# Optimization experiments

Measured on AMD Instinct MI355X. Metric: run time of the kernel, lower is better.

The kernel has to match this reference:

```python
import jax, jax.numpy as jnp
import numpy as np

H = 64  # latent_dim // 2


def _lstm_cell(x, h, c, Wih, Whh, b):
    # PyTorch gate order: i, f, g, o
    g = x @ Wih.T + h @ Whh.T + b
    i, f, gg, o = jnp.split(g, 4, axis=-1)
    c = jax.nn.sigmoid(f) * c + jax.nn.sigmoid(i) * jnp.tanh(gg)
    h = jax.nn.sigmoid(o) * jnp.tanh(c)
    return h, c


def _run_lstm(x, Wih, Whh, b):
    # x: [B, T, D] -> outputs [B, T, H], final h, c (zero-initialized state)
    B = x.shape[0]
    h0 = jnp.zeros((B, Whh.shape[1]), x.dtype)

    def step(carry, xt):
        h, c = _lstm_cell(xt, carry[0], carry[1], Wih, Whh, b)
        return (h, c), h

    (h, c), ys = jax.lax.scan(step, (h0, h0), jnp.swapaxes(x, 0, 1))
    return jnp.swapaxes(ys, 0, 1), h, c


def setup_inputs() -> dict:
    key = jax.random.key(0)
    ks = jax.random.split(key, 16)
    B, S, T, D = 512, 1024, 512, 3
    s = 1.0 / np.sqrt(H)

    def u(k, shape):
        return jax.random.uniform(k, shape, jnp.float32, -s, s)

    return {
        "src": jax.random.normal(ks[0], (B, S, D), jnp.float32),
        "trg": jax.random.normal(ks[1], (B, T, D), jnp.float32),
        "enc1_Wih": u(ks[2], (4 * H, D)),
        "enc1_Whh": u(ks[3], (4 * H, H)),
        "enc1_b": u(ks[4], (4 * H,)),
        "enc2_Wih": u(ks[5], (4 * H, H)),
        "enc2_Whh": u(ks[6], (4 * H, H)),
        "enc2_b": u(ks[7], (4 * H,)),
        "dec1_Wih": u(ks[8], (4 * H, D)),
        "dec1_Whh": u(ks[9], (4 * H, H)),
        "dec1_b": u(ks[10], (4 * H,)),
        "dec2_Wih": u(ks[11], (4 * H, H)),
        "dec2_Whh": u(ks[12], (4 * H, H)),
        "dec2_b": u(ks[13], (4 * H,)),
        "fc_W": u(ks[14], (D, H)),
        "fc_b": u(ks[15], (D,)),
    }


def reference(src, trg, enc1_Wih, enc1_Whh, enc1_b, enc2_Wih, enc2_Whh, enc2_b,
              dec1_Wih, dec1_Whh, dec1_b, dec2_Wih, dec2_Whh, dec2_b, fc_W, fc_b):
    # Encoder: two stacked LSTMs over src; keep final state of layer 2.
    y1, _, _ = _run_lstm(src, enc1_Wih, enc1_Whh, enc1_b)
    _, h, c = _run_lstm(y1, enc2_Wih, enc2_Whh, enc2_b)

    # Decoder (teacher_forcing_ratio = 1.0, the only well-defined branch):
    # at each step both decoder LSTMs share/chain the SAME (h, c) state,
    # exactly as the original Decoder.forward does with seq-len-1 inputs.
    def step(carry, xt):
        h, c = carry
        h1, c1 = _lstm_cell(xt, h, c, dec1_Wih, dec1_Whh, dec1_b)
        h2, c2 = _lstm_cell(h1, h1, c1, dec2_Wih, dec2_Whh, dec2_b)
        return (h2, c2), h2 @ fc_W.T + fc_b

    xs = jnp.swapaxes(trg[:, :-1, :], 0, 1)  # inputs for t = 1..T-1
    _, preds = jax.lax.scan(step, (h, c), xs)
    preds = jnp.swapaxes(preds, 0, 1)  # [B, T-1, 3]

    B = trg.shape[0]
    zero0 = jnp.zeros((B, 1, fc_b.shape[0]), preds.dtype)  # outputs[:, 0] stays 0
    return jnp.concatenate([zero0, preds], axis=1)
```

## Files before the change

kernel.cpp:

```cpp
#include <hip/hip_runtime.h>
#include <math.h>

typedef _Float16 f16;
typedef _Float16 f16x8 __attribute__((ext_vector_type(8)));
typedef float    f32x4 __attribute__((ext_vector_type(4)));

#define MFMA16(A, B, C) __builtin_amdgcn_mfma_f32_16x16x32_f16((A), (B), (C), 0, 0, 0)
#define LOG2E 1.44269504088896f

__device__ __forceinline__ float sig2(float a) {
    return __builtin_amdgcn_rcpf(1.0f + __builtin_amdgcn_exp2f(a));
}
__device__ __forceinline__ float tanh2(float c) {
    return fmaf(2.0f, sig2(c * (-2.0f * LOG2E)), -1.0f);
}

__device__ __forceinline__ f16x8 ldfrag(const float* __restrict__ W, int n, int k0, float s) {
    const float* p = W + (size_t)n * 64 + k0;
    f16x8 r;
#pragma unroll
    for (int j = 0; j < 8; j++) r[j] = (f16)(s * p[j]);
    return r;
}

__global__ __launch_bounds__(512, 2)
void seq2seq_kernel(const float* __restrict__ src, const float* __restrict__ trg,
                    const float* __restrict__ e1ih, const float* __restrict__ e1hh,
                    const float* __restrict__ e1b,
                    const float* __restrict__ e2ih, const float* __restrict__ e2hh,
                    const float* __restrict__ e2b,
                    const float* __restrict__ d1ih, const float* __restrict__ d1hh,
                    const float* __restrict__ d1b,
                    const float* __restrict__ d2ih, const float* __restrict__ d2hh,
                    const float* __restrict__ d2b,
                    const float* __restrict__ fcW, const float* __restrict__ fcb,
                    float* __restrict__ out)
{
    const int bp   = blockIdx.x;
    const int tid  = threadIdx.x;
    const int wv   = tid >> 6;
    const bool isB = (wv >= 4);
    const int wvg  = wv & 3;
    const int lane = tid & 63;
    const int quad = lane >> 4;
    const int c15  = lane & 15;
    const int u16  = wvg * 16 + c15;
    const int qb   = quad & 1;
    const int ab   = c15 & 1;

    __shared__ __align__(16) float xst[1024][8];
    __shared__ __align__(16) float tst[512][8];
    __shared__ __align__(16) f16 h1l[2][2][64];
    __shared__ __align__(16) f16 h2l[2][2][64];
    __shared__ float c1buf[2][64];
    __shared__ float c2buf[2][64];

    {
        const float* s0 = src + (size_t)(2 * bp) * 3072;
        const float* s1 = s0 + 3072;
        for (int i = tid; i < 3072; i += 512) {
            int t = i / 3, c = i - 3 * t;
            xst[t][c]     = s0[i];
            xst[t][4 + c] = s1[i];
        }
        const float* t0p = trg + (size_t)(2 * bp) * 1536;
        const float* t1p = t0p + 1536;
        for (int i = tid; i < 1536; i += 512) {
            int t = i / 3, c = i - 3 * t;
            tst[t][c]     = t0p[i];
            tst[t][4 + c] = t1p[i];
        }
    }

    f16x8 E1hh[4][2];
    f16x8 E2ih[4][2], E2hh[4][2];
    float xw[4][3], bias1[4], bias2[4];
    if (!isB) {
#pragma unroll
        for (int g = 0; g < 4; g++) {
            const float s = (g == 2) ? (-2.0f * LOG2E) : (-LOG2E);
            const int n = g * 64 + u16;
#pragma unroll
            for (int c = 0; c < 2; c++)
                E1hh[g][c] = ldfrag(e1hh, n, c * 32 + quad * 8, s);
            xw[g][0] = s * e1ih[n * 3 + 0];
            xw[g][1] = s * e1ih[n * 3 + 1];
            xw[g][2] = s * e1ih[n * 3 + 2];
            bias1[g] = s * e1b[n];
        }
    } else {
#pragma unroll
        for (int g = 0; g < 4; g++) {
            const float s = (g == 2) ? (-2.0f * LOG2E) : (-LOG2E);
            const int n = g * 64 + u16;
#pragma unroll
            for (int c = 0; c < 2; c++) {
                E2ih[g][c] = ldfrag(e2ih, n, c * 32 + quad * 8, s);
                E2hh[g][c] = ldfrag(e2hh, n, c * 32 + quad * 8, s);
            }
            bias2[g] = s * e2b[n];
        }
    }

    float c1 = 0.f, c2 = 0.f;
    if (tid < 256) {
        (&h1l[0][0][0])[tid] = (f16)0.f;
        (&h2l[0][0][0])[tid] = (f16)0.f;
    }
    __syncthreads();

    const f32x4 z4 = {0.f, 0.f, 0.f, 0.f};

#pragma unroll 1
    for (int tau = 0; tau <= 1024; tau++) {
        const int w = tau & 1;
        if (!isB) {
            if (tau < 1024) {
                const f32x4 xv = *(const f32x4*)&xst[tau][qb * 4];
                const f16* h1p = h1l[w ^ 1][ab];
                f16x8 a0 = *(const f16x8*)(h1p + quad * 8);
                f16x8 a1 = *(const f16x8*)(h1p + 32 + quad * 8);
                float xt[4];
#pragma unroll
                for (int g = 0; g < 4; g++)
                    xt[g] = fmaf(xw[g][0], xv.x,
                            fmaf(xw[g][1], xv.y, fmaf(xw[g][2], xv.z, bias1[g])));
                f32x4 acc[4];
#pragma unroll
                for (int g = 0; g < 4; g++)
                    acc[g] = MFMA16(a1, E1hh[g][1], MFMA16(a0, E1hh[g][0], z4));
                float v[4];
#pragma unroll
                for (int g = 0; g < 4; g++)
                    v[g] = (qb ? acc[g][1] : acc[g][0]) + xt[g];
                float iv = sig2(v[0]), fv = sig2(v[1]);
                float gv = fmaf(2.0f, sig2(v[2]), -1.0f), ov = sig2(v[3]);
                c1 = fv * c1 + iv * gv;
                if (quad < 2) h1l[w][quad][u16] = (f16)(ov * tanh2(c1));
            }
        } else {
            if (tau > 0) {
                const f16* h1p = h1l[w ^ 1][ab];
                const f16* h2p = h2l[w ^ 1][ab];
                f16x8 a0 = *(const f16x8*)(h1p + quad * 8);
                f16x8 a1 = *(const f16x8*)(h1p + 32 + quad * 8);
                f16x8 b0 = *(const f16x8*)(h2p + quad * 8);
                f16x8 b1 = *(const f16x8*)(h2p + 32 + quad * 8);
                f32x4 accA[4], accB[4];
#pragma unroll
                for (int g = 0; g < 4; g++) {
                    accA[g] = MFMA16(a1, E2ih[g][1], MFMA16(a0, E2ih[g][0], z4));
                    accB[g] = MFMA16(b1, E2hh[g][1], MFMA16(b0, E2hh[g][0], z4));
                }
                float v[4];
#pragma unroll
                for (int g = 0; g < 4; g++)
                    v[g] = (qb ? accA[g][1] : accA[g][0]) +
                           (qb ? accB[g][1] : accB[g][0]) + bias2[g];
                float iv = sig2(v[0]), fv = sig2(v[1]);
                float gv = fmaf(2.0f, sig2(v[2]), -1.0f), ov = sig2(v[3]);
                c2 = fv * c2 + iv * gv;
                if (quad < 2) h2l[w][quad][u16] = (f16)(ov * tanh2(c2));
            }
        }
        __syncthreads();
    }

    f16x8 D1hh[4][2];
    f16x8 W2s[4][2];
    float dxw[4][3], db1[4], db2[4];
    if (!isB) {
#pragma unroll
        for (int g = 0; g < 4; g++) {
            const float s = (g == 2) ? (-2.0f * LOG2E) : (-LOG2E);
            const int n = g * 64 + u16;
#pragma unroll
            for (int c = 0; c < 2; c++)
                D1hh[g][c] = ldfrag(d1hh, n, c * 32 + quad * 8, s);
            dxw[g][0] = s * d1ih[n * 3 + 0];
            dxw[g][1] = s * d1ih[n * 3 + 1];
            dxw[g][2] = s * d1ih[n * 3 + 2];
            db1[g] = s * d1b[n];
        }
    } else {
#pragma unroll
        for (int g = 0; g < 4; g++) {
            const float s = (g == 2) ? (-2.0f * LOG2E) : (-LOG2E);
            const int n = g * 64 + u16;
#pragma unroll
            for (int c = 0; c < 2; c++) {
                const int k0 = c * 32 + quad * 8;
                const float* pa = d2ih + (size_t)n * 64 + k0;
                const float* pb = d2hh + (size_t)n * 64 + k0;
                f16x8 r;
#pragma unroll
                for (int j = 0; j < 8; j++) r[j] = (f16)(s * (pa[j] + pb[j]));
                W2s[g][c] = r;
            }
            db2[g] = s * d2b[n];
        }
        if (quad < 2) c2buf[quad][u16] = c2;
    }
    float fw0 = 0.f, fw1 = 0.f, fw2 = 0.f;
    float fb0 = fcb[0], fb1 = fcb[1], fb2 = fcb[2];
    if (wv >= 6) { fw0 = fcW[lane]; fw1 = fcW[64 + lane]; fw2 = fcW[128 + lane]; }
    __syncthreads();

#pragma unroll 1
    for (int t = 0; t < 511; t++) {
        const int r = t & 1, w = r ^ 1;
        if (!isB) {
            const f16* hp = h2l[r][ab];
            f16x8 a0 = *(const f16x8*)(hp + quad * 8);
            f16x8 a1 = *(const f16x8*)(hp + 32 + quad * 8);
            const f32x4 xv = *(const f32x4*)&tst[t][qb * 4];
            float cdin = c2buf[qb][u16];
            float xt[4];
#pragma unroll
            for (int g = 0; g < 4; g++)
                xt[g] = fmaf(dxw[g][0], xv.x,
                        fmaf(dxw[g][1], xv.y, fmaf(dxw[g][2], xv.z, db1[g])));
            f32x4 acc[4];
#pragma unroll
            for (int g = 0; g < 4; g++)
                acc[g] = MFMA16(a1, D1hh[g][1], MFMA16(a0, D1hh[g][0], z4));
            float v[4];
#pragma unroll
            for (int g = 0; g < 4; g++)
                v[g] = (qb ? acc[g][1] : acc[g][0]) + xt[g];
            float iv = sig2(v[0]), fv = sig2(v[1]);
            float gv = fmaf(2.0f, sig2(v[2]), -1.0f), ov = sig2(v[3]);
            float c1d = fv * cdin + iv * gv;
            if (quad < 2) {
                h1l[w][quad][u16] = (f16)(ov * tanh2(c1d));
                c1buf[quad][u16]  = c1d;
            }
        } else if (wv >= 6 && t > 0) {
            const int bsel = wv - 6;
            float hv = (float)h2l[r][bsel][lane];
            float p0 = fw0 * hv, p1 = fw1 * hv, p2 = fw2 * hv;
#pragma unroll
            for (int off = 32; off > 0; off >>= 1) {
                p0 += __shfl_down(p0, off);
                p1 += __shfl_down(p1, off);
                p2 += __shfl_down(p2, off);
            }
            if (lane == 0) {
                float* o = out + ((size_t)(2 * bp + bsel) * 512 + t) * 3;
                o[0] = p0 + fb0; o[1] = p1 + fb1; o[2] = p2 + fb2;
            }
        }
        __syncthreads();

        if (isB) {
            const f16* np = h1l[w][ab];
            f16x8 m0 = *(const f16x8*)(np + quad * 8);
            f16x8 m1 = *(const f16x8*)(np + 32 + quad * 8);
            float c1in = c1buf[qb][u16];
            f32x4 acc[4];
#pragma unroll
            for (int g = 0; g < 4; g++)
                acc[g] = MFMA16(m1, W2s[g][1], MFMA16(m0, W2s[g][0], z4));
            float v[4];
#pragma unroll
            for (int g = 0; g < 4; g++)
                v[g] = (qb ? acc[g][1] : acc[g][0]) + db2[g];
            float i2 = sig2(v[0]), f2 = sig2(v[1]);
            float g2 = fmaf(2.0f, sig2(v[2]), -1.0f), o2 = sig2(v[3]);
            float c2d = f2 * c1in + i2 * g2;
            if (quad < 2) {
                h2l[w][quad][u16] = (f16)(o2 * tanh2(c2d));
                c2buf[quad][u16]  = c2d;
            }
        }
        __syncthreads();
    }

    if (wv >= 6) {
        const int bsel = wv - 6;
        float hv = (float)h2l[1][bsel][lane];
        float p0 = fw0 * hv, p1 = fw1 * hv, p2 = fw2 * hv;
#pragma unroll
        for (int off = 32; off > 0; off >>= 1) {
            p0 += __shfl_down(p0, off);
            p1 += __shfl_down(p1, off);
            p2 += __shfl_down(p2, off);
        }
        if (lane == 0) {
            float* o = out + ((size_t)(2 * bp + bsel) * 512 + 511) * 3;
            o[0] = p0 + fb0; o[1] = p1 + fb1; o[2] = p2 + fb2;
        }
    }
}

extern "C" void kernel_launch(void* const* d_in, const int* in_sizes, int n_in,
                              void* d_out, int out_size, void* d_ws, size_t ws_size,
                              hipStream_t stream)
{
    const float* src   = (const float*)d_in[0];
    const float* trg   = (const float*)d_in[1];
    const float* e1ih  = (const float*)d_in[2];
    const float* e1hh  = (const float*)d_in[3];
    const float* e1b   = (const float*)d_in[4];
    const float* e2ih  = (const float*)d_in[5];
    const float* e2hh  = (const float*)d_in[6];
    const float* e2b   = (const float*)d_in[7];
    const float* dd1ih = (const float*)d_in[8];
    const float* dd1hh = (const float*)d_in[9];
    const float* dd1b  = (const float*)d_in[10];
    const float* dd2ih = (const float*)d_in[11];
    const float* dd2hh = (const float*)d_in[12];
    const float* dd2b  = (const float*)d_in[13];
    const float* fcW   = (const float*)d_in[14];
    const float* fcb   = (const float*)d_in[15];
    float* out = (float*)d_out;

    hipMemsetAsync(d_out, 0, (size_t)out_size * sizeof(float), stream);

    seq2seq_kernel<<<256, 512, 0, stream>>>(src, trg,
                                            e1ih, e1hh, e1b, e2ih, e2hh, e2b,
                                            dd1ih, dd1hh, dd1b, dd2ih, dd2hh, dd2b,
                                            fcW, fcb, out);
}
```

Measured before the change: 926.0 us.

## Batch FC output via ring buffer MFMA, prefetch inputs, fold biases into MFMA

Decoder h2 outputs are written into a 16-step shared ring buffer, and the final linear layer is computed every 16 steps with one MFMA instead of a per-step shuffle reduction. Next-step input features are prefetched into registers before the barrier. Layer-2 biases are folded into the MFMA accumulator initialisation. This cuts per-step latency on the serial critical path but adds an fp16 FC projection and more complex indexing at the boundaries.

```diff
diff --git a/kernel.cpp b/kernel.cpp
--- a/kernel.cpp
+++ b/kernel.cpp
@@ -54,6 +54,7 @@
     __shared__ __align__(16) f16 h2l[2][2][64];
     __shared__ float c1buf[2][64];
     __shared__ float c2buf[2][64];
+    __shared__ __align__(16) f16 ring[2][16][72];
 
     {
         const float* s0 = src + (size_t)(2 * bp) * 3072;
@@ -74,7 +75,8 @@
 
     f16x8 E1hh[4][2];
     f16x8 E2ih[4][2], E2hh[4][2];
-    float xw[4][3], bias1[4], bias2[4];
+    float xw[4][3], bias1[4];
+    f32x4 bs2[4];
     if (!isB) {
 #pragma unroll
         for (int g = 0; g < 4; g++) {
@@ -98,7 +100,8 @@
                 E2ih[g][c] = ldfrag(e2ih, n, c * 32 + quad * 8, s);
                 E2hh[g][c] = ldfrag(e2hh, n, c * 32 + quad * 8, s);
             }
-            bias2[g] = s * e2b[n];
+            float bv = s * e2b[n];
+            bs2[g] = (f32x4){bv, bv, bv, bv};
         }
     }
 
@@ -110,21 +113,23 @@
     __syncthreads();
 
     const f32x4 z4 = {0.f, 0.f, 0.f, 0.f};
+
+    f32x4 xq = z4, xnq = z4;
+    if (!isB) xq = *(const f32x4*)&xst[0][qb * 4];
 
 #pragma unroll 1
     for (int tau = 0; tau <= 1024; tau++) {
         const int w = tau & 1;
         if (!isB) {
             if (tau < 1024) {
-                const f32x4 xv = *(const f32x4*)&xst[tau][qb * 4];
                 const f16* h1p = h1l[w ^ 1][ab];
                 f16x8 a0 = *(const f16x8*)(h1p + quad * 8);
                 f16x8 a1 = *(const f16x8*)(h1p + 32 + quad * 8);
                 float xt[4];
 #pragma unroll
                 for (int g = 0; g < 4; g++)
-                    xt[g] = fmaf(xw[g][0], xv.x,
-                            fmaf(xw[g][1], xv.y, fmaf(xw[g][2], xv.z, bias1[g])));
+                    xt[g] = fmaf(xw[g][0], xq.x,
+                            fmaf(xw[g][1], xq.y, fmaf(xw[g][2], xq.z, bias1[g])));
                 f32x4 acc[4];
 #pragma unroll
                 for (int g = 0; g < 4; g++)
@@ -137,6 +142,8 @@
                 float gv = fmaf(2.0f, sig2(v[2]), -1.0f), ov = sig2(v[3]);
                 c1 = fv * c1 + iv * gv;
                 if (quad < 2) h1l[w][quad][u16] = (f16)(ov * tanh2(c1));
+                const int tn = (tau + 1 < 1024) ? tau + 1 : 1023;
+                xnq = *(const f32x4*)&xst[tn][qb * 4];
             }
         } else {
             if (tau > 0) {
@@ -149,14 +156,14 @@
                 f32x4 accA[4], accB[4];
 #pragma unroll
                 for (int g = 0; g < 4; g++) {
-                    accA[g] = MFMA16(a1, E2ih[g][1], MFMA16(a0, E2ih[g][0], z4));
+                    accA[g] = MFMA16(a1, E2ih[g][1], MFMA16(a0, E2ih[g][0], bs2[g]));
                     accB[g] = MFMA16(b1, E2hh[g][1], MFMA16(b0, E2hh[g][0], z4));
                 }
                 float v[4];
 #pragma unroll
                 for (int g = 0; g < 4; g++)
                     v[g] = (qb ? accA[g][1] : accA[g][0]) +
-                           (qb ? accB[g][1] : accB[g][0]) + bias2[g];
+                           (qb ? accB[g][1] : accB[g][0]);
                 float iv = sig2(v[0]), fv = sig2(v[1]);
                 float gv = fmaf(2.0f, sig2(v[2]), -1.0f), ov = sig2(v[3]);
                 c2 = fv * c2 + iv * gv;
@@ -164,11 +171,13 @@
             }
         }
         __syncthreads();
+        if (!isB) xq = xnq;
     }
 
     f16x8 D1hh[4][2];
     f16x8 W2s[4][2];
-    float dxw[4][3], db1[4], db2[4];
+    float dxw[4][3], db1[4];
+    f32x4 db2s[4];
     if (!isB) {
 #pragma unroll
         for (int g = 0; g < 4; g++) {
@@ -197,14 +206,25 @@
                 for (int j = 0; j < 8; j++) r[j] = (f16)(s * (pa[j] + pb[j]));
                 W2s[g][c] = r;
             }
-            db2[g] = s * d2b[n];
+            float bv = s * d2b[n];
+            db2s[g] = (f32x4){bv, bv, bv, bv};
         }
         if (quad < 2) c2buf[quad][u16] = c2;
     }
-    float fw0 = 0.f, fw1 = 0.f, fw2 = 0.f;
-    float fb0 = fcb[0], fb1 = fcb[1], fb2 = fcb[2];
-    if (wv >= 6) { fw0 = fcW[lane]; fw1 = fcW[64 + lane]; fw2 = fcW[128 + lane]; }
+    f16x8 FW0 = {}, FW1 = {};
+    float fb = 0.f;
+    if (wv >= 6 && c15 < 3) {
+#pragma unroll
+        for (int j = 0; j < 8; j++) {
+            FW0[j] = (f16)fcW[c15 * 64 + quad * 8 + j];
+            FW1[j] = (f16)fcW[c15 * 64 + 32 + quad * 8 + j];
+        }
+        fb = fcb[c15];
+    }
     __syncthreads();
+
+    f32x4 tq = z4, tnq = z4;
+    if (!isB) tq = *(const f32x4*)&tst[0][qb * 4];
 
 #pragma unroll 1
     for (int t = 0; t < 511; t++) {
@@ -213,13 +233,12 @@
             const f16* hp = h2l[r][ab];
             f16x8 a0 = *(const f16x8*)(hp + quad * 8);
             f16x8 a1 = *(const f16x8*)(hp + 32 + quad * 8);
-            const f32x4 xv = *(const f32x4*)&tst[t][qb * 4];
             float cdin = c2buf[qb][u16];
             float xt[4];
 #pragma unroll
             for (int g = 0; g < 4; g++)
-                xt[g] = fmaf(dxw[g][0], xv.x,
-                        fmaf(dxw[g][1], xv.y, fmaf(dxw[g][2], xv.z, db1[g])));
+                xt[g] = fmaf(dxw[g][0], tq.x,
+                        fmaf(dxw[g][1], tq.y, fmaf(dxw[g][2], tq.z, db1[g])));
             f32x4 acc[4];
 #pragma unroll
             for (int g = 0; g < 4; g++)
@@ -235,22 +254,23 @@
                 h1l[w][quad][u16] = (f16)(ov * tanh2(c1d));
                 c1buf[quad][u16]  = c1d;
             }
-        } else if (wv >= 6 && t > 0) {
+            const int tn = (t + 1 < 511) ? t + 1 : 510;
+            tnq = *(const f32x4*)&tst[tn][qb * 4];
+        } else if (wv >= 6 && t > 0 && (t & 15) == 0) {
             const int bsel = wv - 6;
-            float hv = (float)h2l[r][bsel][lane];
-            float p0 = fw0 * hv, p1 = fw1 * hv, p2 = fw2 * hv;
-#pragma unroll
-            for (int off = 32; off > 0; off >>= 1) {
-                p0 += __shfl_down(p0, off);
-                p1 += __shfl_down(p1, off);
-                p2 += __shfl_down(p2, off);
-            }
-            if (lane == 0) {
-                float* o = out + ((size_t)(2 * bp + bsel) * 512 + t) * 3;
-                o[0] = p0 + fb0; o[1] = p1 + fb1; o[2] = p2 + fb2;
+            const f16* rp = &ring[bsel][0][0];
+            f16x8 fa0 = *(const f16x8*)(rp + c15 * 72 + quad * 8);
+            f16x8 fa1 = *(const f16x8*)(rp + c15 * 72 + 32 + quad * 8);
+            f32x4 acc = MFMA16(fa1, FW1, MFMA16(fa0, FW0, z4));
+            if (c15 < 3) {
+                float* ob = out + (((size_t)(2 * bp + bsel) * 512 + (t - 15)) * 3) + c15;
+#pragma unroll
+                for (int rg = 0; rg < 4; rg++)
+                    ob[(quad * 4 + rg) * 3] = acc[rg] + fb;
             }
         }
         __syncthreads();
+        if (!isB) tq = tnq;
 
         if (isB) {
             const f16* np = h1l[w][ab];
@@ -260,17 +280,19 @@
             f32x4 acc[4];
 #pragma unroll
             for (int g = 0; g < 4; g++)
-                acc[g] = MFMA16(m1, W2s[g][1], MFMA16(m0, W2s[g][0], z4));
+                acc[g] = MFMA16(m1, W2s[g][1], MFMA16(m0, W2s[g][0], db2s[g]));
             float v[4];
 #pragma unroll
             for (int g = 0; g < 4; g++)
-                v[g] = (qb ? acc[g][1] : acc[g][0]) + db2[g];
+                v[g] = (qb ? acc[g][1] : acc[g][0]);
             float i2 = sig2(v[0]), f2 = sig2(v[1]);
             float g2 = fmaf(2.0f, sig2(v[2]), -1.0f), o2 = sig2(v[3]);
             float c2d = f2 * c1in + i2 * g2;
             if (quad < 2) {
-                h2l[w][quad][u16] = (f16)(o2 * tanh2(c2d));
+                f16 hh = (f16)(o2 * tanh2(c2d));
+                h2l[w][quad][u16] = hh;
                 c2buf[quad][u16]  = c2d;
+                ring[quad][t & 15][u16] = hh;
             }
         }
         __syncthreads();
@@ -278,17 +300,17 @@
 
     if (wv >= 6) {
         const int bsel = wv - 6;
-        float hv = (float)h2l[1][bsel][lane];
-        float p0 = fw0 * hv, p1 = fw1 * hv, p2 = fw2 * hv;
-#pragma unroll
-        for (int off = 32; off > 0; off >>= 1) {
-            p0 += __shfl_down(p0, off);
-            p1 += __shfl_down(p1, off);
-            p2 += __shfl_down(p2, off);
-        }
-        if (lane == 0) {
-            float* o = out + ((size_t)(2 * bp + bsel) * 512 + 511) * 3;
-            o[0] = p0 + fb0; o[1] = p1 + fb1; o[2] = p2 + fb2;
+        const f16* rp = &ring[bsel][0][0];
+        f16x8 fa0 = *(const f16x8*)(rp + c15 * 72 + quad * 8);
+        f16x8 fa1 = *(const f16x8*)(rp + c15 * 72 + 32 + quad * 8);
+        f32x4 acc = MFMA16(fa1, FW1, MFMA16(fa0, FW0, z4));
+        if (c15 < 3) {
+            float* ob = out + (((size_t)(2 * bp + bsel) * 512 + 497) * 3) + c15;
+#pragma unroll
+            for (int rg = 0; rg < 4; rg++) {
+                int step = quad * 4 + rg;
+                if (step < 15) ob[step * 3] = acc[rg] + fb;
+            }
         }
     }
 }
```

After: 834.8 us (median of 2 runs). -9.8%, faster.
